# Optimization experiments

Hardware: AMD Instinct MI355X
Metric: run time of the kernel (lower is better)

## Reference

```python
import jax, jax.numpy as jnp
import numpy as np

N, T, S, H, HC, LMH = 100, 2, 6, 64, 64, 128  # zones, timesteps, state, actor/critic GRU hidden, localized hidden
MAX_ACTION = 3.0
NB = (S + 1) * 5  # 35: neighbor-concat feature size


def setup_inputs() -> dict:
    key = jax.random.key(0)
    ks = iter(jax.random.split(key, 40))
    def rn(shape, s=0.05):
        return jax.random.normal(next(ks), shape, dtype=jnp.float32) * s
    B = 2048
    return {
        "x": jax.random.normal(next(ks), (B, T, N, S), dtype=jnp.float32),
        # 100 independent SubActor parameter sets, stacked along leading unit axis
        "a_Wih": rn((N, 3 * H, S)), "a_Whh": rn((N, 3 * H, H)),
        "a_bih": rn((N, 3 * H)), "a_bhh": rn((N, 3 * H)),
        "a_W1": rn((N, H, H)), "a_b1": rn((N, H)),
        "a_W2": rn((N, H, H)), "a_b2": rn((N, H)),
        "a_W3": rn((N, 1, H)), "a_b3": rn((N, 1)),
        # LocalizedModule 99 (only index 99 survives the buggy critic loop)
        "lm_W1": rn((LMH, NB)), "lm_b1": rn((LMH,)),
        "lm_W2": rn((LMH, LMH)), "lm_b2": rn((LMH,)),
        "lm_W3": rn((1, LMH)), "lm_b3": rn((1,)),
        # SubCritic 99
        "sc_Wih": rn((3 * HC, NB)), "sc_Whh": rn((3 * HC, HC)),
        "sc_bih": rn((3 * HC,)), "sc_bhh": rn((3 * HC,)),
        "sc_W1": rn((HC, HC)), "sc_b1": rn((HC,)),
        "sc_W2": rn((HC, HC)), "sc_b2": rn((HC,)),
        "sc_W3": rn((1, HC)), "sc_b3": rn((1,)),
    }


def _gru_cell(gx, gh, h):
    # PyTorch GRU gate order: r, z, n
    xr, xz, xn = jnp.split(gx, 3, axis=-1)
    hr, hz, hn = jnp.split(gh, 3, axis=-1)
    r = jax.nn.sigmoid(xr + hr)
    z = jax.nn.sigmoid(xz + hz)
    n = jnp.tanh(xn + r * hn)
    return (1.0 - z) * n + z * h


def _forward(x, a_Wih, a_Whh, a_bih, a_bhh, a_W1, a_b1, a_W2, a_b2, a_W3, a_b3,
             lm_W1, lm_b1, lm_W2, lm_b2, lm_W3, lm_b3,
             sc_Wih, sc_Whh, sc_bih, sc_bhh, sc_W1, sc_b1, sc_W2, sc_b2, sc_W3, sc_b3):
    B = x.shape[0]
    # ---- ActorNetwork: 100 independent GRU+MLP units, batched over unit axis n ----
    gx = jnp.einsum('btns,ngs->btng', x, a_Wih) + a_bih  # [B,T,N,3H]
    def astep(h, gx_t):
        gh = jnp.einsum('bnh,ngh->bng', h, a_Whh) + a_bhh
        h2 = _gru_cell(gx_t, gh, h)
        return h2, h2
    h0 = jnp.zeros((B, N, H), x.dtype)
    _, hs = jax.lax.scan(astep, h0, jnp.moveaxis(gx, 1, 0))
    hseq = jnp.moveaxis(hs, 0, 1)  # [B,T,N,H]
    a = jax.nn.relu(hseq)
    a = jax.nn.relu(jnp.einsum('btnh,nkh->btnk', a, a_W1) + a_b1)
    a = jax.nn.relu(jnp.einsum('btnh,nkh->btnk', a, a_W2) + a_b2)
    a = MAX_ACTION * (jax.nn.sigmoid(jnp.einsum('btnh,nkh->btnk', a, a_W3) + a_b3) - 0.5)  # [B,T,N,1]
    # torch.stack over units -> (N,B,T,1), then .view(-1,T,N): subactor-major flat reinterpretation
    p = jnp.transpose(a[..., 0], (2, 0, 1)).reshape(B, T, N)
    xc = jnp.concatenate([x, p[..., None]], axis=-1)  # [B,T,N,S+1]
    # ---- CriticNetwork: f/q lists are reset inside the loop, so only i=99 contributes ----
    # neighbors of 99: (99, 89, 100->zeros, 109->zeros, 98)
    z7 = jnp.zeros_like(xc[:, :, 99])
    xi = jnp.concatenate([xc[:, :, 99], xc[:, :, 89], z7, z7, xc[:, :, 98]], axis=-1)  # [B,T,35]
    # LocalizedModule 99 on last timestep
    f = jax.nn.relu(xi[:, -1] @ lm_W1.T + lm_b1)
    f = jax.nn.relu(f @ lm_W2.T + lm_b2)
    f = f @ lm_W3.T + lm_b3  # [B,1]
    # SubCritic 99: GRU then per-timestep MLP; only last timestep is returned,
    # and the MLP is per-timestep, so applying it to the last hidden state is exact.
    cgx = xi @ sc_Wih.T + sc_bih  # [B,T,3HC]
    def cstep(h, gx_t):
        gh = h @ sc_Whh.T + sc_bhh
        h2 = _gru_cell(gx_t, gh, h)
        return h2, h2
    h_last, _ = jax.lax.scan(cstep, jnp.zeros((B, HC), x.dtype), jnp.moveaxis(cgx, 1, 0))
    c = jax.nn.relu(h_last)
    c = jax.nn.relu(c @ sc_W1.T + sc_b1)
    c = jax.nn.relu(c @ sc_W2.T + sc_b2)
    q = c @ sc_W3.T + sc_b3  # [B,1]
    q_total = jnp.sum(f + q, axis=1)  # [B]
    return p[:, -1], q_total.reshape(-1, 1)


def reference(x, a_Wih, a_Whh, a_bih, a_bhh, a_W1, a_b1, a_W2, a_b2, a_W3, a_b3,
              lm_W1, lm_b1, lm_W2, lm_b2, lm_W3, lm_b3,
              sc_Wih, sc_Whh, sc_bih, sc_bhh, sc_W1, sc_b1, sc_W2, sc_b2, sc_W3, sc_b3):
    return _forward(x, a_Wih, a_Whh, a_bih, a_bhh, a_W1, a_b1, a_W2, a_b2, a_W3, a_b3,
                    lm_W1, lm_b1, lm_W2, lm_b2, lm_W3, lm_b3,
                    sc_Wih, sc_Whh, sc_bih, sc_bhh, sc_W1, sc_b1, sc_W2, sc_b2, sc_W3, sc_b3)
```

## Files before the change

### kernel.cpp

```cpp
#include <hip/hip_runtime.h>
#include <hip/hip_bf16.h>

typedef __attribute__((ext_vector_type(8))) short short8;
typedef __attribute__((ext_vector_type(4))) float f32x4;

#define SLAB 44032
#define WS_W_OFF 1638400

#define OFF_X 44032
#define OFF_H 48128
#define OFF_A 64512
#define LDS_TOTAL 80896

__device__ __forceinline__ unsigned pkbf(float a, float b) {
    __hip_bfloat162 h = __float22bfloat162_rn(make_float2(a, b));
    return *reinterpret_cast<unsigned*>(&h);
}
__device__ __forceinline__ float sigf(float x) {
    return __builtin_amdgcn_rcpf(1.f + __builtin_amdgcn_exp2f(-1.4426950408889634f * x));
}
__device__ __forceinline__ float tanhfast(float y) {
    return 1.f - 2.f * __builtin_amdgcn_rcpf(1.f + __builtin_amdgcn_exp2f(2.8853900817779268f * y));
}
__device__ __forceinline__ void g2l16(const void* g, void* l) {
    __builtin_amdgcn_global_load_lds(
        (const __attribute__((address_space(1))) void*)g,
        (__attribute__((address_space(3))) void*)l, 16, 0, 0);
}

__global__ __launch_bounds__(256)
void convert_kernel(const float* __restrict__ Wih, const float* __restrict__ Whh,
                    const float* __restrict__ W1, const float* __restrict__ W2,
                    char* __restrict__ slab)
{
    int idx = blockIdx.x * 256 + threadIdx.x;
    if (idx >= 100 * 11008) return;
    int n = idx / 11008;
    int i = idx - n * 11008;
    char* zs = slab + (size_t)n * SLAB;
    if (i < 768) {
        int row = i >> 2, j = i & 3;
        const float* g = Wih + n * 1152 + row * 6;
        float a = (2 * j < 6) ? g[2 * j] : 0.f;
        float b = (2 * j + 1 < 6) ? g[2 * j + 1] : 0.f;
        *(unsigned*)(zs + row * 16 + j * 4) = pkbf(a, b);
    } else if (i < 6912) {
        int k = i - 768, row = k >> 5, j = k & 31;
        float2 v = *(const float2*)(Whh + n * 12288 + row * 64 + j * 2);
        *(unsigned*)(zs + 3072 + row * 128 + ((j * 4) ^ ((row & 7) << 4))) = pkbf(v.x, v.y);
    } else if (i < 8960) {
        int k = i - 6912, row = k >> 5, j = k & 31;
        float2 v = *(const float2*)(W1 + n * 4096 + row * 64 + j * 2);
        *(unsigned*)(zs + 27648 + row * 128 + ((j * 4) ^ ((row & 7) << 4))) = pkbf(v.x, v.y);
    } else {
        int k = i - 8960, row = k >> 5, j = k & 31;
        float2 v = *(const float2*)(W2 + n * 4096 + row * 64 + j * 2);
        *(unsigned*)(zs + 35840 + row * 128 + ((j * 4) ^ ((row & 7) << 4))) = pkbf(v.x, v.y);
    }
}

__global__ __launch_bounds__(256, 2)
void actor_kernel(const float* __restrict__ x, const char* __restrict__ slab,
                  const float* __restrict__ bih, const float* __restrict__ bhh,
                  const float* __restrict__ b1, const float* __restrict__ b2,
                  const float* __restrict__ W3, const float* __restrict__ b3,
                  float* __restrict__ p_flat)
{
    extern __shared__ char sm[];
    const int tid   = threadIdx.x;
    const int n     = blockIdx.x >> 4;
    const int chunk = blockIdx.x & 15;
    const int w     = tid >> 6;
    const int l     = tid & 63;
    const int bcol  = l & 15;
    const int grp   = l >> 4;
    const int a7    = bcol & 7;
    const int ch0   = grp * 4;

    {
        const char* gz = slab + (size_t)n * SLAB;
        for (int i = w; i < 43; i += 4)
            g2l16(gz + i * 1024 + l * 16, sm + i * 1024);
        int t = tid >> 7, b = tid & 127;
        const float* xr = x + (size_t)(chunk * 128 + b) * 1200 + t * 600 + n * 6;
        uint4 pk;
        pk.x = pkbf(xr[0], xr[1]);
        pk.y = pkbf(xr[2], xr[3]);
        pk.z = pkbf(xr[4], xr[5]);
        pk.w = 0u;
        *(uint4*)(sm + OFF_X + (t * 128 + b) * 16) = pk;
    }
    __syncthreads();

    const int gsz = (grp ^ a7) << 4;
    const char* wihp = sm + bcol * 16;
    const char* whhA = sm + 3072  + bcol * 128 + gsz;
    const char* whhB = sm + 3072  + bcol * 128 + (gsz ^ 64);
    const char* w1A  = sm + 27648 + bcol * 128 + gsz;
    const char* w1B  = sm + 27648 + bcol * 128 + (gsz ^ 64);
    const char* w2A  = sm + 35840 + bcol * 128 + gsz;
    const char* w2B  = sm + 35840 + bcol * 128 + (gsz ^ 64);
    char* hTile = sm + OFF_H + w * 4096;
    char* aTile = sm + OFF_A + w * 4096;
    const int wgr = (grp & 1) * 8;
    const int g1v = grp >> 1;

    const float* bihz = bih + n * 192;
    const float* bhhz = bhh + n * 192;
    f32x4 bRi[4], bZi[4], bXNi[4], bHNi[4];
#pragma unroll
    for (int mt = 0; mt < 4; ++mt) {
        const int ch = mt * 16 + ch0;
        bRi[mt]  = *(const f32x4*)&bihz[ch]      + *(const f32x4*)&bhhz[ch];
        bZi[mt]  = *(const f32x4*)&bihz[64 + ch] + *(const f32x4*)&bhhz[64 + ch];
        bXNi[mt] = *(const f32x4*)&bihz[128 + ch];
        bHNi[mt] = *(const f32x4*)&bhhz[128 + ch];
    }
    const float b3v = b3[n];
    const short8 zfrag = {0, 0, 0, 0, 0, 0, 0, 0};

    f32x4 hp[2][4];
#pragma unroll
    for (int nt = 0; nt < 2; ++nt)
#pragma unroll
        for (int mt = 0; mt < 4; ++mt) hp[nt][mt] = (f32x4){0.f, 0.f, 0.f, 0.f};

    for (int t = 0; t < 2; ++t) {
        short8 bxv[2] = {zfrag, zfrag};
        if (grp == 0) {
            bxv[0] = *(const short8*)(sm + OFF_X + (t * 128 + w * 32 + bcol) * 16);
            bxv[1] = *(const short8*)(sm + OFF_X + (t * 128 + w * 32 + 16 + bcol) * 16);
        }
        short8 bh0v[2], bh1v[2];
        if (t == 1) {
#pragma unroll
            for (int nt = 0; nt < 2; ++nt) {
                bh0v[nt] = *(const short8*)(hTile + (nt * 16 + bcol) * 128 + gsz);
                bh1v[nt] = *(const short8*)(hTile + (nt * 16 + bcol) * 128 + (gsz ^ 64));
            }
        }
#pragma unroll
        for (int mt = 0; mt < 4; ++mt) {
            f32x4 aR[2], aZ[2], aXN[2], aHN[2];
#pragma unroll
            for (int nt = 0; nt < 2; ++nt) {
                aR[nt] = bRi[mt]; aZ[nt] = bZi[mt]; aXN[nt] = bXNi[mt]; aHN[nt] = bHNi[mt];
            }
            short8 wr = zfrag, wzg = zfrag, wn = zfrag;
            if (grp == 0) {
                wr  = *(const short8*)(wihp + (0 + mt) * 256);
                wzg = *(const short8*)(wihp + (4 + mt) * 256);
                wn  = *(const short8*)(wihp + (8 + mt) * 256);
            }
#pragma unroll
            for (int nt = 0; nt < 2; ++nt) {
                aR[nt]  = __builtin_amdgcn_mfma_f32_16x16x32_bf16(wr,  bxv[nt], aR[nt],  0, 0, 0);
                aZ[nt]  = __builtin_amdgcn_mfma_f32_16x16x32_bf16(wzg, bxv[nt], aZ[nt],  0, 0, 0);
                aXN[nt] = __builtin_amdgcn_mfma_f32_16x16x32_bf16(wn,  bxv[nt], aXN[nt], 0, 0, 0);
            }
            if (t == 1) {
                short8 r0 = *(const short8*)(whhA + (0 + mt) * 2048);
                short8 r1 = *(const short8*)(whhB + (0 + mt) * 2048);
                short8 z0 = *(const short8*)(whhA + (4 + mt) * 2048);
                short8 z1 = *(const short8*)(whhB + (4 + mt) * 2048);
                short8 n0 = *(const short8*)(whhA + (8 + mt) * 2048);
                short8 n1 = *(const short8*)(whhB + (8 + mt) * 2048);
#pragma unroll
                for (int nt = 0; nt < 2; ++nt) {
                    aR[nt]  = __builtin_amdgcn_mfma_f32_16x16x32_bf16(r0, bh0v[nt], aR[nt],  0, 0, 0);
                    aR[nt]  = __builtin_amdgcn_mfma_f32_16x16x32_bf16(r1, bh1v[nt], aR[nt],  0, 0, 0);
                    aZ[nt]  = __builtin_amdgcn_mfma_f32_16x16x32_bf16(z0, bh0v[nt], aZ[nt],  0, 0, 0);
                    aZ[nt]  = __builtin_amdgcn_mfma_f32_16x16x32_bf16(z1, bh1v[nt], aZ[nt],  0, 0, 0);
                    aHN[nt] = __builtin_amdgcn_mfma_f32_16x16x32_bf16(n0, bh0v[nt], aHN[nt], 0, 0, 0);
                    aHN[nt] = __builtin_amdgcn_mfma_f32_16x16x32_bf16(n1, bh1v[nt], aHN[nt], 0, 0, 0);
                }
            }
#pragma unroll
            for (int nt = 0; nt < 2; ++nt) {
                f32x4 h2;
#pragma unroll
                for (int r = 0; r < 4; ++r) {
                    float rg = sigf(aR[nt][r]);
                    float zg = sigf(aZ[nt][r]);
                    float nn = tanhfast(aXN[nt][r] + rg * aHN[nt][r]);
                    h2[r] = nn + zg * (hp[nt][mt][r] - nn);
                }
                hp[nt][mt] = h2;
                char* wmt = hTile + nt * 2048 + bcol * 128 + wgr + (((2 * mt + g1v) ^ a7) << 4);
                if (t == 0) {
                    uint2 ph; ph.x = pkbf(h2[0], h2[1]); ph.y = pkbf(h2[2], h2[3]);
                    *(uint2*)wmt = ph;
                }
                uint2 pa;
                pa.x = pkbf(fmaxf(h2[0], 0.f), fmaxf(h2[1], 0.f));
                pa.y = pkbf(fmaxf(h2[2], 0.f), fmaxf(h2[3], 0.f));
                *(uint2*)(wmt + 16384) = pa;
            }
        }
        {
            short8 ba0[2], ba1[2];
#pragma unroll
            for (int nt = 0; nt < 2; ++nt) {
                ba0[nt] = *(const short8*)(aTile + (nt * 16 + bcol) * 128 + gsz);
                ba1[nt] = *(const short8*)(aTile + (nt * 16 + bcol) * 128 + (gsz ^ 64));
            }
#pragma unroll
            for (int mt = 0; mt < 4; ++mt) {
                short8 wa  = *(const short8*)(w1A + mt * 2048);
                short8 wbv = *(const short8*)(w1B + mt * 2048);
                f32x4 bmv = *(const f32x4*)&b1[n * 64 + mt * 16 + ch0];
#pragma unroll
                for (int nt = 0; nt < 2; ++nt) {
                    f32x4 m1 = bmv;
                    m1 = __builtin_amdgcn_mfma_f32_16x16x32_bf16(wa,  ba0[nt], m1, 0, 0, 0);
                    m1 = __builtin_amdgcn_mfma_f32_16x16x32_bf16(wbv, ba1[nt], m1, 0, 0, 0);
                    uint2 pm;
                    pm.x = pkbf(fmaxf(m1[0], 0.f), fmaxf(m1[1], 0.f));
                    pm.y = pkbf(fmaxf(m1[2], 0.f), fmaxf(m1[3], 0.f));
                    *(uint2*)(aTile + nt * 2048 + bcol * 128 + wgr + (((2 * mt + g1v) ^ a7) << 4)) = pm;
                }
            }
        }
        {
            short8 bm0[2], bm1[2];
#pragma unroll
            for (int nt = 0; nt < 2; ++nt) {
                bm0[nt] = *(const short8*)(aTile + (nt * 16 + bcol) * 128 + gsz);
                bm1[nt] = *(const short8*)(aTile + (nt * 16 + bcol) * 128 + (gsz ^ 64));
            }
            float part[2] = {0.f, 0.f};
#pragma unroll
            for (int mt = 0; mt < 4; ++mt) {
                short8 wa  = *(const short8*)(w2A + mt * 2048);
                short8 wbv = *(const short8*)(w2B + mt * 2048);
                f32x4 bmv = *(const f32x4*)&b2[n * 64 + mt * 16 + ch0];
                f32x4 w3v = *(const f32x4*)&W3[n * 64 + mt * 16 + ch0];
#pragma unroll
                for (int nt = 0; nt < 2; ++nt) {
                    f32x4 m2 = bmv;
                    m2 = __builtin_amdgcn_mfma_f32_16x16x32_bf16(wa,  bm0[nt], m2, 0, 0, 0);
                    m2 = __builtin_amdgcn_mfma_f32_16x16x32_bf16(wbv, bm1[nt], m2, 0, 0, 0);
#pragma unroll
                    for (int r = 0; r < 4; ++r)
                        part[nt] += w3v[r] * fmaxf(m2[r], 0.f);
                }
            }
#pragma unroll
            for (int nt = 0; nt < 2; ++nt) {
                part[nt] += __shfl_xor(part[nt], 16, 64);
                part[nt] += __shfl_xor(part[nt], 32, 64);
            }
            if (l < 16) {
#pragma unroll
                for (int nt = 0; nt < 2; ++nt) {
                    int bg = chunk * 128 + w * 32 + nt * 16 + bcol;
                    float val = 3.f * (sigf(part[nt] + b3v) - 0.5f);
                    p_flat[n * 4096 + bg * 2 + t] = val;
                }
            }
        }
    }
}

__global__ __launch_bounds__(256, 2)
void critic_kernel(const float* __restrict__ x, const float* __restrict__ p_flat,
                   const float* __restrict__ lmW1, const float* __restrict__ lmb1,
                   const float* __restrict__ lmW2, const float* __restrict__ lmb2,
                   const float* __restrict__ lmW3, const float* __restrict__ lmb3,
                   const float* __restrict__ scWih, const float* __restrict__ scWhh,
                   const float* __restrict__ scbih, const float* __restrict__ scbhh,
                   const float* __restrict__ scW1, const float* __restrict__ scb1,
                   const float* __restrict__ scW2, const float* __restrict__ scb2,
                   const float* __restrict__ scW3, const float* __restrict__ scb3,
                   float* __restrict__ out)
{
    __shared__ float sxi[4][72];
    __shared__ float shh[4][68];
    __shared__ float sab[4][68];
    __shared__ float sc1[4][68];
    __shared__ float sf1[4][132];

    const int tid = threadIdx.x;
    const int wid = tid >> 6;
    const int lane = tid & 63;
    const int b = blockIdx.x * 4 + wid;

    for (int idx = lane; idx < 72; idx += 64) {
        int t = idx / 36, c = idx - t * 36;
        float v = 0.f;
        if (c < 35) {
            int g = c / 7, e = c - g * 7;
            int z = (g == 0) ? 99 : (g == 1) ? 89 : (g == 4) ? 98 : -1;
            if (z >= 0)
                v = (e < 6) ? x[((size_t)b * 2 + t) * 600 + z * 6 + e]
                            : p_flat[b * 200 + t * 100 + z];
        }
        sxi[wid][idx] = v;
    }
    __syncthreads();

    float cg00 = scbih[lane], cg01 = scbih[lane + 64], cg02 = scbih[lane + 128];
    float cg10 = cg00, cg11 = cg01, cg12 = cg02;
    for (int c = 0; c < 35; ++c) {
        float w0 = scWih[lane * 35 + c];
        float w1 = scWih[(lane + 64) * 35 + c];
        float w2 = scWih[(lane + 128) * 35 + c];
        float x0 = sxi[wid][c], x1 = sxi[wid][36 + c];
        cg00 += w0 * x0; cg01 += w1 * x0; cg02 += w2 * x0;
        cg10 += w0 * x1; cg11 += w1 * x1; cg12 += w2 * x1;
    }
    const float bhr = scbhh[lane], bhz = scbhh[lane + 64], bhn = scbhh[lane + 128];
    float r  = 1.f / (1.f + expf(-(cg00 + bhr)));
    float zg = 1.f / (1.f + expf(-(cg01 + bhz)));
    float nn = tanhf(cg02 + r * bhn);
    float hj = (1.f - zg) * nn;
    shh[wid][lane] = hj;
    __syncthreads();
    float ghr = bhr, ghz = bhz, ghn = bhn;
    for (int kc = 0; kc < 16; ++kc) {
        float4 wr  = *(const float4*)&scWhh[lane * 64 + kc * 4];
        float4 wzv = *(const float4*)&scWhh[(lane + 64) * 64 + kc * 4];
        float4 wn  = *(const float4*)&scWhh[(lane + 128) * 64 + kc * 4];
        float4 hv  = *(const float4*)&shh[wid][kc * 4];
        ghr += wr.x * hv.x + wr.y * hv.y + wr.z * hv.z + wr.w * hv.w;
        ghz += wzv.x * hv.x + wzv.y * hv.y + wzv.z * hv.z + wzv.w * hv.w;
        ghn += wn.x * hv.x + wn.y * hv.y + wn.z * hv.z + wn.w * hv.w;
    }
    r  = 1.f / (1.f + expf(-(cg10 + ghr)));
    zg = 1.f / (1.f + expf(-(cg11 + ghz)));
    nn = tanhf(cg12 + r * ghn);
    hj = (1.f - zg) * nn + zg * hj;
    sab[wid][lane] = fmaxf(hj, 0.f);
    __syncthreads();
    float acc = scb1[lane];
    for (int kc = 0; kc < 16; ++kc) {
        float4 wv = *(const float4*)&scW1[lane * 64 + kc * 4];
        float4 av = *(const float4*)&sab[wid][kc * 4];
        acc += wv.x * av.x + wv.y * av.y + wv.z * av.z + wv.w * av.w;
    }
    sc1[wid][lane] = fmaxf(acc, 0.f);
    __syncthreads();
    float acc2 = scb2[lane];
    for (int kc = 0; kc < 16; ++kc) {
        float4 wv = *(const float4*)&scW2[lane * 64 + kc * 4];
        float4 av = *(const float4*)&sc1[wid][kc * 4];
        acc2 += wv.x * av.x + wv.y * av.y + wv.z * av.z + wv.w * av.w;
    }
    float qpart = scW3[lane] * fmaxf(acc2, 0.f);
    float f1a = lmb1[lane], f1c = lmb1[lane + 64];
    for (int c = 0; c < 35; ++c) {
        float xv = sxi[wid][36 + c];
        f1a += lmW1[lane * 35 + c] * xv;
        f1c += lmW1[(lane + 64) * 35 + c] * xv;
    }
    sf1[wid][lane] = fmaxf(f1a, 0.f);
    sf1[wid][lane + 64] = fmaxf(f1c, 0.f);
    __syncthreads();
    float f2a = lmb2[lane], f2c = lmb2[lane + 64];
    for (int kc = 0; kc < 32; ++kc) {
        float4 fv = *(const float4*)&sf1[wid][kc * 4];
        float4 wa = *(const float4*)&lmW2[lane * 128 + kc * 4];
        float4 wc = *(const float4*)&lmW2[(lane + 64) * 128 + kc * 4];
        f2a += wa.x * fv.x + wa.y * fv.y + wa.z * fv.z + wa.w * fv.w;
        f2c += wc.x * fv.x + wc.y * fv.y + wc.z * fv.z + wc.w * fv.w;
    }
    float fpart = lmW3[lane] * fmaxf(f2a, 0.f) + lmW3[lane + 64] * fmaxf(f2c, 0.f);

    float tot = qpart + fpart;
    for (int m = 32; m > 0; m >>= 1) tot += __shfl_xor(tot, m, 64);
    if (lane == 0) out[204800 + b] = tot + scb3[0] + lmb3[0];

    for (int l2 = lane; l2 < 100; l2 += 64)
        out[b * 100 + l2] = p_flat[b * 200 + 100 + l2];
}

extern "C" void kernel_launch(void* const* d_in, const int* in_sizes, int n_in,
                              void* d_out, int out_size, void* d_ws, size_t ws_size,
                              hipStream_t stream) {
    const float* x     = (const float*)d_in[0];
    const float* aWih  = (const float*)d_in[1];
    const float* aWhh  = (const float*)d_in[2];
    const float* abih  = (const float*)d_in[3];
    const float* abhh  = (const float*)d_in[4];
    const float* aW1   = (const float*)d_in[5];
    const float* ab1   = (const float*)d_in[6];
    const float* aW2   = (const float*)d_in[7];
    const float* ab2   = (const float*)d_in[8];
    const float* aW3   = (const float*)d_in[9];
    const float* ab3   = (const float*)d_in[10];
    const float* lmW1  = (const float*)d_in[11];
    const float* lmb1  = (const float*)d_in[12];
    const float* lmW2  = (const float*)d_in[13];
    const float* lmb2  = (const float*)d_in[14];
    const float* lmW3  = (const float*)d_in[15];
    const float* lmb3  = (const float*)d_in[16];
    const float* scWih = (const float*)d_in[17];
    const float* scWhh = (const float*)d_in[18];
    const float* scbih = (const float*)d_in[19];
    const float* scbhh = (const float*)d_in[20];
    const float* scW1  = (const float*)d_in[21];
    const float* scb1  = (const float*)d_in[22];
    const float* scW2  = (const float*)d_in[23];
    const float* scb2  = (const float*)d_in[24];
    const float* scW3  = (const float*)d_in[25];
    const float* scb3  = (const float*)d_in[26];
    float* out = (float*)d_out;
    float* p_flat = (float*)d_ws;
    char* slab = (char*)d_ws + WS_W_OFF;

    hipFuncSetAttribute((const void*)actor_kernel,
                        hipFuncAttributeMaxDynamicSharedMemorySize, LDS_TOTAL);

    convert_kernel<<<dim3((100 * 11008 + 255) / 256), 256, 0, stream>>>(
        aWih, aWhh, aW1, aW2, slab);

    actor_kernel<<<dim3(1600), 256, LDS_TOTAL, stream>>>(
        x, slab, abih, abhh, ab1, ab2, aW3, ab3, p_flat);

    critic_kernel<<<dim3(512), 256, 0, stream>>>(
        x, p_flat, lmW1, lmb1, lmW2, lmb2, lmW3, lmb3,
        scWih, scWhh, scbih, scbhh, scW1, scb1, scW2, scb2, scW3, scb3, out);
}
```

Baseline: 96.05 us.

## Double actor block batch and register-tile critic over four rows per wave

The actor kernel now uses 512-thread blocks covering 256 batch rows per zone, so each staged weight slab in LDS serves twice as many rows and half as many blocks are launched. The critic kernel has each wave process four batch rows, reusing every global weight load across those rows and dropping block-wide barriers, since each wave only touches its own rows. This cuts redundant weight traffic, but it raises LDS use per block, which lowers resident-block flexibility, and it raises register pressure in the critic. The critic grid also shrinks to 128 blocks, which reduces parallelism.

```diff
diff --git a/kernel.cpp b/kernel.cpp
--- a/kernel.cpp
+++ b/kernel.cpp
@@ -8,9 +8,9 @@
 #define WS_W_OFF 1638400
 
 #define OFF_X 44032
-#define OFF_H 48128
-#define OFF_A 64512
-#define LDS_TOTAL 80896
+#define OFF_H 52224
+#define OFF_A 84992
+#define LDS_TOTAL 117760
 
 __device__ __forceinline__ unsigned pkbf(float a, float b) {
     __hip_bfloat162 h = __float22bfloat162_rn(make_float2(a, b));
@@ -59,7 +59,7 @@
     }
 }
 
-__global__ __launch_bounds__(256, 2)
+__global__ __launch_bounds__(512, 2)
 void actor_kernel(const float* __restrict__ x, const char* __restrict__ slab,
                   const float* __restrict__ bih, const float* __restrict__ bhh,
                   const float* __restrict__ b1, const float* __restrict__ b2,
@@ -68,8 +68,8 @@
 {
     extern __shared__ char sm[];
     const int tid   = threadIdx.x;
-    const int n     = blockIdx.x >> 4;
-    const int chunk = blockIdx.x & 15;
+    const int n     = blockIdx.x >> 3;
+    const int chunk = blockIdx.x & 7;
     const int w     = tid >> 6;
     const int l     = tid & 63;
     const int bcol  = l & 15;
@@ -79,16 +79,16 @@
 
     {
         const char* gz = slab + (size_t)n * SLAB;
-        for (int i = w; i < 43; i += 4)
+        for (int i = w; i < 43; i += 8)
             g2l16(gz + i * 1024 + l * 16, sm + i * 1024);
-        int t = tid >> 7, b = tid & 127;
-        const float* xr = x + (size_t)(chunk * 128 + b) * 1200 + t * 600 + n * 6;
+        int t = tid >> 8, b = tid & 255;
+        const float* xr = x + (size_t)(chunk * 256 + b) * 1200 + t * 600 + n * 6;
         uint4 pk;
         pk.x = pkbf(xr[0], xr[1]);
         pk.y = pkbf(xr[2], xr[3]);
         pk.z = pkbf(xr[4], xr[5]);
         pk.w = 0u;
-        *(uint4*)(sm + OFF_X + (t * 128 + b) * 16) = pk;
+        *(uint4*)(sm + OFF_X + (t * 256 + b) * 16) = pk;
     }
     __syncthreads();
 
@@ -128,8 +128,8 @@
     for (int t = 0; t < 2; ++t) {
         short8 bxv[2] = {zfrag, zfrag};
         if (grp == 0) {
-            bxv[0] = *(const short8*)(sm + OFF_X + (t * 128 + w * 32 + bcol) * 16);
-            bxv[1] = *(const short8*)(sm + OFF_X + (t * 128 + w * 32 + 16 + bcol) * 16);
+            bxv[0] = *(const short8*)(sm + OFF_X + (t * 256 + w * 32 + bcol) * 16);
+            bxv[1] = *(const short8*)(sm + OFF_X + (t * 256 + w * 32 + 16 + bcol) * 16);
         }
         short8 bh0v[2], bh1v[2];
         if (t == 1) {
@@ -194,7 +194,7 @@
                 uint2 pa;
                 pa.x = pkbf(fmaxf(h2[0], 0.f), fmaxf(h2[1], 0.f));
                 pa.y = pkbf(fmaxf(h2[2], 0.f), fmaxf(h2[3], 0.f));
-                *(uint2*)(wmt + 16384) = pa;
+                *(uint2*)(wmt + 32768) = pa;
             }
         }
         {
@@ -253,7 +253,7 @@
             if (l < 16) {
 #pragma unroll
                 for (int nt = 0; nt < 2; ++nt) {
-                    int bg = chunk * 128 + w * 32 + nt * 16 + bcol;
+                    int bg = chunk * 256 + w * 32 + nt * 16 + bcol;
                     float val = 3.f * (sigf(part[nt] + b3v) - 0.5f);
                     p_flat[n * 4096 + bg * 2 + t] = val;
                 }
@@ -274,104 +274,153 @@
                    const float* __restrict__ scW3, const float* __restrict__ scb3,
                    float* __restrict__ out)
 {
-    __shared__ float sxi[4][72];
-    __shared__ float shh[4][68];
-    __shared__ float sab[4][68];
-    __shared__ float sc1[4][68];
-    __shared__ float sf1[4][132];
+    __shared__ float sxi[16][72];
+    __shared__ float shh[16][68];
+    __shared__ float sab[16][68];
+    __shared__ float sc1[16][68];
+    __shared__ float sf1[16][132];
 
     const int tid = threadIdx.x;
     const int wid = tid >> 6;
     const int lane = tid & 63;
-    const int b = blockIdx.x * 4 + wid;
-
-    for (int idx = lane; idx < 72; idx += 64) {
-        int t = idx / 36, c = idx - t * 36;
+    const int b0 = blockIdx.x * 16 + wid * 4;
+
+    for (int idx = lane; idx < 288; idx += 64) {
+        int r = idx / 72, k = idx - r * 72;
+        int t = k / 36, c = k - t * 36;
         float v = 0.f;
         if (c < 35) {
             int g = c / 7, e = c - g * 7;
             int z = (g == 0) ? 99 : (g == 1) ? 89 : (g == 4) ? 98 : -1;
             if (z >= 0)
-                v = (e < 6) ? x[((size_t)b * 2 + t) * 600 + z * 6 + e]
-                            : p_flat[b * 200 + t * 100 + z];
-        }
-        sxi[wid][idx] = v;
+                v = (e < 6) ? x[((size_t)(b0 + r) * 2 + t) * 600 + z * 6 + e]
+                            : p_flat[(b0 + r) * 200 + t * 100 + z];
+        }
+        sxi[wid * 4 + r][k] = v;
     }
     __syncthreads();
 
-    float cg00 = scbih[lane], cg01 = scbih[lane + 64], cg02 = scbih[lane + 128];
-    float cg10 = cg00, cg11 = cg01, cg12 = cg02;
+    const float bir = scbih[lane], biz = scbih[lane + 64], bin = scbih[lane + 128];
+    float cr0[4], cz0[4], cn0[4], cr1[4], cz1[4], cn1[4];
+#pragma unroll
+    for (int r = 0; r < 4; ++r) {
+        cr0[r] = bir; cz0[r] = biz; cn0[r] = bin;
+        cr1[r] = bir; cz1[r] = biz; cn1[r] = bin;
+    }
     for (int c = 0; c < 35; ++c) {
         float w0 = scWih[lane * 35 + c];
         float w1 = scWih[(lane + 64) * 35 + c];
         float w2 = scWih[(lane + 128) * 35 + c];
-        float x0 = sxi[wid][c], x1 = sxi[wid][36 + c];
-        cg00 += w0 * x0; cg01 += w1 * x0; cg02 += w2 * x0;
-        cg10 += w0 * x1; cg11 += w1 * x1; cg12 += w2 * x1;
+#pragma unroll
+        for (int r = 0; r < 4; ++r) {
+            float x0 = sxi[wid * 4 + r][c], x1 = sxi[wid * 4 + r][36 + c];
+            cr0[r] += w0 * x0; cz0[r] += w1 * x0; cn0[r] += w2 * x0;
+            cr1[r] += w0 * x1; cz1[r] += w1 * x1; cn1[r] += w2 * x1;
+        }
     }
     const float bhr = scbhh[lane], bhz = scbhh[lane + 64], bhn = scbhh[lane + 128];
-    float r  = 1.f / (1.f + expf(-(cg00 + bhr)));
-    float zg = 1.f / (1.f + expf(-(cg01 + bhz)));
-    float nn = tanhf(cg02 + r * bhn);
-    float hj = (1.f - zg) * nn;
-    shh[wid][lane] = hj;
-    __syncthreads();
-    float ghr = bhr, ghz = bhz, ghn = bhn;
+    float hj[4];
+#pragma unroll
+    for (int r = 0; r < 4; ++r) {
+        float rg = 1.f / (1.f + expf(-(cr0[r] + bhr)));
+        float zg = 1.f / (1.f + expf(-(cz0[r] + bhz)));
+        float nn = tanhf(cn0[r] + rg * bhn);
+        hj[r] = (1.f - zg) * nn;
+        shh[wid * 4 + r][lane] = hj[r];
+    }
+    float ghr[4], ghz[4], ghn[4];
+#pragma unroll
+    for (int r = 0; r < 4; ++r) { ghr[r] = bhr; ghz[r] = bhz; ghn[r] = bhn; }
     for (int kc = 0; kc < 16; ++kc) {
         float4 wr  = *(const float4*)&scWhh[lane * 64 + kc * 4];
         float4 wzv = *(const float4*)&scWhh[(lane + 64) * 64 + kc * 4];
         float4 wn  = *(const float4*)&scWhh[(lane + 128) * 64 + kc * 4];
-        float4 hv  = *(const float4*)&shh[wid][kc * 4];
-        ghr += wr.x * hv.x + wr.y * hv.y + wr.z * hv.z + wr.w * hv.w;
-        ghz += wzv.x * hv.x + wzv.y * hv.y + wzv.z * hv.z + wzv.w * hv.w;
-        ghn += wn.x * hv.x + wn.y * hv.y + wn.z * hv.z + wn.w * hv.w;
-    }
-    r  = 1.f / (1.f + expf(-(cg10 + ghr)));
-    zg = 1.f / (1.f + expf(-(cg11 + ghz)));
-    nn = tanhf(cg12 + r * ghn);
-    hj = (1.f - zg) * nn + zg * hj;
-    sab[wid][lane] = fmaxf(hj, 0.f);
-    __syncthreads();
-    float acc = scb1[lane];
+#pragma unroll
+        for (int r = 0; r < 4; ++r) {
+            float4 hv = *(const float4*)&shh[wid * 4 + r][kc * 4];
+            ghr[r] += wr.x * hv.x + wr.y * hv.y + wr.z * hv.z + wr.w * hv.w;
+            ghz[r] += wzv.x * hv.x + wzv.y * hv.y + wzv.z * hv.z + wzv.w * hv.w;
+            ghn[r] += wn.x * hv.x + wn.y * hv.y + wn.z * hv.z + wn.w * hv.w;
+        }
+    }
+#pragma unroll
+    for (int r = 0; r < 4; ++r) {
+        float rg = 1.f / (1.f + expf(-(cr1[r] + ghr[r])));
+        float zg = 1.f / (1.f + expf(-(cz1[r] + ghz[r])));
+        float nn = tanhf(cn1[r] + rg * ghn[r]);
+        hj[r] = (1.f - zg) * nn + zg * hj[r];
+        sab[wid * 4 + r][lane] = fmaxf(hj[r], 0.f);
+    }
+    float acc[4];
+#pragma unroll
+    for (int r = 0; r < 4; ++r) acc[r] = scb1[lane];
     for (int kc = 0; kc < 16; ++kc) {
         float4 wv = *(const float4*)&scW1[lane * 64 + kc * 4];
-        float4 av = *(const float4*)&sab[wid][kc * 4];
-        acc += wv.x * av.x + wv.y * av.y + wv.z * av.z + wv.w * av.w;
-    }
-    sc1[wid][lane] = fmaxf(acc, 0.f);
-    __syncthreads();
-    float acc2 = scb2[lane];
+#pragma unroll
+        for (int r = 0; r < 4; ++r) {
+            float4 av = *(const float4*)&sab[wid * 4 + r][kc * 4];
+            acc[r] += wv.x * av.x + wv.y * av.y + wv.z * av.z + wv.w * av.w;
+        }
+    }
+#pragma unroll
+    for (int r = 0; r < 4; ++r) sc1[wid * 4 + r][lane] = fmaxf(acc[r], 0.f);
+    float qpart[4];
+#pragma unroll
+    for (int r = 0; r < 4; ++r) acc[r] = scb2[lane];
     for (int kc = 0; kc < 16; ++kc) {
         float4 wv = *(const float4*)&scW2[lane * 64 + kc * 4];
-        float4 av = *(const float4*)&sc1[wid][kc * 4];
-        acc2 += wv.x * av.x + wv.y * av.y + wv.z * av.z + wv.w * av.w;
-    }
-    float qpart = scW3[lane] * fmaxf(acc2, 0.f);
-    float f1a = lmb1[lane], f1c = lmb1[lane + 64];
+#pragma unroll
+        for (int r = 0; r < 4; ++r) {
+            float4 av = *(const float4*)&sc1[wid * 4 + r][kc * 4];
+            acc[r] += wv.x * av.x + wv.y * av.y + wv.z * av.z + wv.w * av.w;
+        }
+    }
+    const float w3l = scW3[lane];
+#pragma unroll
+    for (int r = 0; r < 4; ++r) qpart[r] = w3l * fmaxf(acc[r], 0.f);
+    float f1a[4], f1c[4];
+#pragma unroll
+    for (int r = 0; r < 4; ++r) { f1a[r] = lmb1[lane]; f1c[r] = lmb1[lane + 64]; }
     for (int c = 0; c < 35; ++c) {
-        float xv = sxi[wid][36 + c];
-        f1a += lmW1[lane * 35 + c] * xv;
-        f1c += lmW1[(lane + 64) * 35 + c] * xv;
-    }
-    sf1[wid][lane] = fmaxf(f1a, 0.f);
-    sf1[wid][lane + 64] = fmaxf(f1c, 0.f);
-    __syncthreads();
-    float f2a = lmb2[lane], f2c = lmb2[lane + 64];
+        float wa = lmW1[lane * 35 + c];
+        float wc = lmW1[(lane + 64) * 35 + c];
+#pragma unroll
+        for (int r = 0; r < 4; ++r) {
+            float xv = sxi[wid * 4 + r][36 + c];
+            f1a[r] += wa * xv;
+            f1c[r] += wc * xv;
+        }
+    }
+#pragma unroll
+    for (int r = 0; r < 4; ++r) {
+        sf1[wid * 4 + r][lane] = fmaxf(f1a[r], 0.f);
+        sf1[wid * 4 + r][lane + 64] = fmaxf(f1c[r], 0.f);
+    }
+    float f2a[4], f2c[4];
+#pragma unroll
+    for (int r = 0; r < 4; ++r) { f2a[r] = lmb2[lane]; f2c[r] = lmb2[lane + 64]; }
     for (int kc = 0; kc < 32; ++kc) {
-        float4 fv = *(const float4*)&sf1[wid][kc * 4];
         float4 wa = *(const float4*)&lmW2[lane * 128 + kc * 4];
         float4 wc = *(const float4*)&lmW2[(lane + 64) * 128 + kc * 4];
-        f2a += wa.x * fv.x + wa.y * fv.y + wa.z * fv.z + wa.w * fv.w;
-        f2c += wc.x * fv.x + wc.y * fv.y + wc.z * fv.z + wc.w * fv.w;
-    }
-    float fpart = lmW3[lane] * fmaxf(f2a, 0.f) + lmW3[lane + 64] * fmaxf(f2c, 0.f);
-
-    float tot = qpart + fpart;
-    for (int m = 32; m > 0; m >>= 1) tot += __shfl_xor(tot, m, 64);
-    if (lane == 0) out[204800 + b] = tot + scb3[0] + lmb3[0];
-
-    for (int l2 = lane; l2 < 100; l2 += 64)
-        out[b * 100 + l2] = p_flat[b * 200 + 100 + l2];
+#pragma unroll
+        for (int r = 0; r < 4; ++r) {
+            float4 fv = *(const float4*)&sf1[wid * 4 + r][kc * 4];
+            f2a[r] += wa.x * fv.x + wa.y * fv.y + wa.z * fv.z + wa.w * fv.w;
+            f2c[r] += wc.x * fv.x + wc.y * fv.y + wc.z * fv.z + wc.w * fv.w;
+        }
+    }
+    const float w3a = lmW3[lane], w3c = lmW3[lane + 64];
+#pragma unroll
+    for (int r = 0; r < 4; ++r) {
+        float tot = qpart[r] + w3a * fmaxf(f2a[r], 0.f) + w3c * fmaxf(f2c[r], 0.f);
+        for (int m = 32; m > 0; m >>= 1) tot += __shfl_xor(tot, m, 64);
+        if (lane == 0) out[204800 + b0 + r] = tot + scb3[0] + lmb3[0];
+    }
+
+#pragma unroll
+    for (int r = 0; r < 4; ++r)
+        for (int l2 = lane; l2 < 100; l2 += 64)
+            out[(b0 + r) * 100 + l2] = p_flat[(b0 + r) * 200 + 100 + l2];
 }
 
 extern "C" void kernel_launch(void* const* d_in, const int* in_sizes, int n_in,
@@ -414,10 +463,10 @@
     convert_kernel<<<dim3((100 * 11008 + 255) / 256), 256, 0, stream>>>(
         aWih, aWhh, aW1, aW2, slab);
 
-    actor_kernel<<<dim3(1600), 256, LDS_TOTAL, stream>>>(
+    actor_kernel<<<dim3(800), 512, LDS_TOTAL, stream>>>(
         x, slab, abih, abhh, ab1, ab2, aW3, ab3, p_flat);
 
-    critic_kernel<<<dim3(512), 256, 0, stream>>>(
+    critic_kernel<<<dim3(128), 256, 0, stream>>>(
         x, p_flat, lmW1, lmb1, lmW2, lmb2, lmW3, lmb3,
         scWih, scWhh, scbih, scbhh, scW1, scb1, scW2, scb2, scW3, scb3, out);
 }
```

Result: slower. 113.0 us (+17.6%).
